# Performance work log

Measured on AMD Instinct MI355X. Metric: run time of the kernel, lower is better.

Reference implementation:

```python
import jax, jax.numpy as jnp
import numpy as np

N = 30000      # nodes
E = 480000     # edges (before self-loops)
D = 100        # hidden_dim / in_channels
H = 4          # heads
PH = 100       # per-head dim
L = 6          # layers
G = 128        # graphs in batch
NUM_ATOM = 100
OUT_DIM = 64


def _xavier(k, shape, gain=1.0):
    fan_in, fan_out = shape[-1], shape[-2]
    lim = gain * np.sqrt(6.0 / (fan_in + fan_out))
    return jax.random.uniform(k, shape, jnp.float32, -lim, lim)


def setup_inputs() -> dict:
    key = jax.random.key(0)
    ks = jax.random.split(key, 12)
    x = jax.random.randint(ks[0], (N,), 0, NUM_ATOM)
    edge_index = jax.random.randint(ks[1], (2, E), 0, N)
    edge_attr = jax.random.normal(ks[2], (E, D), dtype=jnp.float32)
    batch = jnp.sort(jax.random.randint(ks[3], (N,), 0, G))
    emb = _xavier(ks[4], (NUM_ATOM, D))
    W = _xavier(ks[5], (L, H * PH, D))
    We = _xavier(ks[6], (L, H * PH, D))
    a = _xavier(ks[7], (L, H, 2 * PH), gain=1.414)
    ln_g = jnp.ones((L, D), jnp.float32)
    ln_b = jnp.zeros((L, D), jnp.float32)
    w1 = _xavier(ks[8], (OUT_DIM, D))
    b1 = jnp.zeros((OUT_DIM,), jnp.float32)
    w2 = _xavier(ks[9], (1, OUT_DIM))
    b2 = jnp.zeros((1,), jnp.float32)
    return dict(x=x, edge_index=edge_index, edge_attr=edge_attr, batch=batch,
                emb=emb, W=W, We=We, a=a, ln_g=ln_g, ln_b=ln_b,
                w1=w1, b1=b1, w2=w2, b2=b2)


def _forward(x, edge_index, edge_attr, batch, emb, W, We, a, ln_g, ln_b, w1, b1, w2, b2):
    n = x.shape[0]
    loop = jnp.arange(n)
    src = jnp.concatenate([edge_index[0], loop])            # [E']
    dst = jnp.concatenate([edge_index[1], loop])            # [E']  (target, softmax key)
    ea = jnp.concatenate([edge_attr, jnp.zeros((n, D), edge_attr.dtype)], axis=0)  # self-loop attr = 0
    h = emb[x]                                              # [N, D]
    for l in range(L):
        hx = (h @ W[l].T).reshape(n, H, PH)                 # [N, H, PH]
        he = (ea @ We[l].T).reshape(-1, H, PH)              # [E', H, PH]
        a_i, a_j = a[l][:, :PH], a[l][:, PH:]               # [H, PH] each
        # alpha = sum(a * [x_i ; x_j + edge_attr]) split into two dots
        score_i = jnp.einsum('nhd,hd->nh', hx, a_i)         # [N, H]
        xj = hx[src]                                        # [E', H, PH]
        alpha = score_i[dst] + jnp.einsum('ehd,hd->eh', xj + he, a_j)  # [E', H]
        alpha = jnp.where(alpha > 0, alpha, 0.2 * alpha)    # leaky_relu(0.2)
        # segment softmax over edges grouped by target node (every node has a self-loop)
        amax = jax.ops.segment_max(alpha, dst, num_segments=n)
        alpha = jnp.exp(alpha - amax[dst])
        denom = jax.ops.segment_sum(alpha, dst, num_segments=n)
        alpha = alpha / (denom[dst] + 1e-16)
        msg = (xj * alpha[..., None]).sum(axis=1)           # [E', PH] (heads summed, per module)
        aggr = jax.ops.segment_sum(msg, dst, num_segments=n)  # [N, PH]
        # LayerNorm(D), eps=1e-5
        mu = aggr.mean(-1, keepdims=True)
        var = ((aggr - mu) ** 2).mean(-1, keepdims=True)
        y = (aggr - mu) / jnp.sqrt(var + 1e-5) * ln_g[l] + ln_b[l]
        y = jax.nn.elu(y)                                   # dropout = identity (eval)
        h = y + h
    # global mean pool over graphs
    s = jax.ops.segment_sum(h, batch, num_segments=G)
    cnt = jax.ops.segment_sum(jnp.ones((n, 1), h.dtype), batch, num_segments=G)
    pooled = s / jnp.maximum(cnt, 1.0)
    hh = pooled @ w1.T + b1                                 # [G, 64]
    out = hh @ w2.T + b2                                    # [G, 1]
    return out, hh


def reference(x, edge_index, edge_attr, batch, emb, W, We, a, ln_g, ln_b, w1, b1, w2, b2):
    return _forward(x, edge_index, edge_attr, batch, emb, W, We, a, ln_g, ln_b, w1, b1, w2, b2)
```

## Files before the change

kernel.cpp:

```cpp
#include <hip/hip_runtime.h>
#include <cstdint>
#include <cstddef>

#define N_NODES 30000
#define N_EDGES 480000
#define EP_EDGES (N_EDGES + N_NODES)
#define DIM 100
#define NH 4
#define NL 6
#define NG 128
#define KP 416

#define OFF_H       0u
#define OFF_AGG2    12000000u
#define OFF_EID     12000000u
#define OFF_DEG     14040000u
#define OFF_CURS    14160000u
#define OFF_ETMP    16000000u
#define OFF_POOL    12000000u
#define OFF_CNT     12051200u
#define OFF_H16     40000000u
#define OFF_SCI     60000000u
#define OFF_SCJ     60480000u
#define OFF_ESC     60960000u
#define OFF_CWIJ    85440000u
#define OFF_WR      85469184u
#define OFF_INDPTR  86429184u
#define OFF_CSRS    86549248u
#define OFF_BSUM    88589248u
#define OFF_BW      88589376u

typedef _Float16 half8 __attribute__((ext_vector_type(8)));
typedef __fp16 fp16x2 __attribute__((ext_vector_type(2)));
typedef float f32x4 __attribute__((ext_vector_type(4)));

static __device__ __forceinline__ unsigned short f2h(float f) {
  return __builtin_bit_cast(unsigned short, (_Float16)f);
}
static __device__ __forceinline__ float h2f(unsigned short u) {
  return (float)__builtin_bit_cast(_Float16, u);
}

__global__ __launch_bounds__(256) void k_init(const int* __restrict__ x,
                                              const float* __restrict__ emb,
                                              float* __restrict__ h,
                                              unsigned short* __restrict__ h16,
                                              int* __restrict__ deg, int* __restrict__ cursor) {
  int tid = blockIdx.x * 256 + threadIdx.x;
  if (tid < N_NODES * DIM) {
    int n = tid / DIM;
    int d = tid - n * DIM;
    float v = emb[x[n] * DIM + d];
    h[tid] = v;
    h16[tid] = f2h(v);
  }
  if (tid < N_NODES) { deg[tid] = 0; cursor[tid] = 0; }
}

__global__ __launch_bounds__(256) void k_fold(const float* __restrict__ W,
                                              const float* __restrict__ We,
                                              const float* __restrict__ a,
                                              float* __restrict__ cWij,
                                              unsigned short* __restrict__ Bw) {
  int tid = blockIdx.x * 256 + threadIdx.x;
  if (tid < NL * DIM * 8) {
    int l = tid / 800, r = tid % 800;
    int k = r >> 3, c = r & 7;
    int hh = c & 3, isJ = c >> 2;
    const float* wp = W + (size_t)(l * 400 + hh * 100) * 100 + k;
    const float* ap = a + (size_t)(l * 4 + hh) * 200 + isJ * 100;
    float s = 0.f;
    for (int d = 0; d < 100; ++d) s += wp[(size_t)d * 100] * ap[d];
    cWij[l * 800 + k * 8 + c] = s;
  } else if (tid < NL * DIM * 8 + DIM * 24) {
    int m = tid - NL * DIM * 8;
    int k = m / 24, c = m % 24;
    int l = c >> 2, hh = c & 3;
    const float* wp = We + (size_t)(l * 400 + hh * 100) * 100 + k;
    const float* ap = a + (size_t)(l * 4 + hh) * 200 + 100;
    float s = 0.f;
    for (int d = 0; d < 100; ++d) s += wp[(size_t)d * 100] * ap[d];
    _Float16 vh = (_Float16)s;
    _Float16 vl = (_Float16)(s - (float)vh);
    int ct = c >> 4;
    int lane = (((k & 31) >> 3) << 4) | (c & 15);
    int ks = k >> 5;
    int j = k & 7;
    Bw[(size_t)(((0 * 2 + ct) * 4 + ks) * 64 + lane) * 8 + j] = __builtin_bit_cast(unsigned short, vh);
    Bw[(size_t)(((1 * 2 + ct) * 4 + ks) * 64 + lane) * 8 + j] = __builtin_bit_cast(unsigned short, vl);
  } else if (tid < NL * DIM * 8 + DIM * 24 + 8192) {
    int E = tid - (NL * DIM * 8 + DIM * 24);
    int j = E & 7;
    int lane = (E >> 3) & 63;
    int rest = E >> 9;
    int ks = rest & 3;
    int ct = (rest >> 2) & 1;
    int c = ct * 16 + (lane & 15);
    int k = ks * 32 + ((lane >> 4) << 3) + j;
    if (!(c < 24 && k < 100)) Bw[E] = 0;
  }
}

__global__ __launch_bounds__(256) void k_bfrag(const float* __restrict__ W,
                                               unsigned short* __restrict__ Bfrag) {
  int tid = blockIdx.x * 256 + threadIdx.x;
  if (tid >= NL * 7 * 13 * 64 * 8) return;
  int j = tid & 7;
  int lane = (tid >> 3) & 63;
  int rest = tid >> 9;
  int ks = rest % 13;
  int rest2 = rest / 13;
  int ct = rest2 % 7;
  int l = rest2 / 7;
  int k = ks * 32 + ((lane >> 4) << 3) + j;
  int n = ct * 16 + (lane & 15);
  float v = 0.f;
  if (k < 400 && n < 100) {
    int hh = k / 100, kk = k - hh * 100;
    v = W[(size_t)(l * 400 + hh * 100 + n) * 100 + kk];
  }
  Bfrag[tid] = f2h(v);
}

__global__ __launch_bounds__(256) void k_deg(const int* __restrict__ ei, int* __restrict__ deg) {
  int tid = blockIdx.x * 256 + threadIdx.x;
  if (tid >= EP_EDGES) return;
  int dstn = (tid < N_EDGES) ? ei[N_EDGES + tid] : (tid - N_EDGES);
  atomicAdd(&deg[dstn], 1);
}

__global__ __launch_bounds__(1024) void k_scan1(const int* __restrict__ deg,
                                                int* __restrict__ indptr, int* __restrict__ bsum) {
  __shared__ int s[1024];
  int t = threadIdx.x;
  int i = blockIdx.x * 1024 + t;
  int v = (i < N_NODES) ? deg[i] : 0;
  s[t] = v;
  __syncthreads();
  for (int off = 1; off < 1024; off <<= 1) {
    int tmp = (t >= off) ? s[t - off] : 0;
    __syncthreads();
    s[t] += tmp;
    __syncthreads();
  }
  if (i < N_NODES) indptr[i + 1] = s[t];
  if (t == 1023) bsum[blockIdx.x] = s[1023];
}
__global__ __launch_bounds__(64) void k_scan2(int* __restrict__ bsum) {
  int t = threadIdx.x;
  int v = (t < 30) ? bsum[t] : 0;
  int inc = v;
  for (int off = 1; off < 64; off <<= 1) {
    int up = __shfl_up(inc, off);
    if (t >= off) inc += up;
  }
  if (t < 30) bsum[t] = inc - v;
}
__global__ __launch_bounds__(1024) void k_scan3(int* __restrict__ indptr,
                                                const int* __restrict__ bsum) {
  int i = blockIdx.x * 1024 + threadIdx.x;
  if (i < N_NODES) indptr[i + 1] += bsum[blockIdx.x];
  if (i == 0) indptr[0] = 0;
}

__global__ __launch_bounds__(256) void k_scatter(const int* __restrict__ ei,
                                                 const int* __restrict__ indptr,
                                                 int* __restrict__ cursor,
                                                 int* __restrict__ csr_src,
                                                 int* __restrict__ csr_eid) {
  int tid = blockIdx.x * 256 + threadIdx.x;
  if (tid >= EP_EDGES) return;
  int dstn = (tid < N_EDGES) ? ei[N_EDGES + tid] : (tid - N_EDGES);
  int srcn = (tid < N_EDGES) ? ei[tid] : (tid - N_EDGES);
  int p = indptr[dstn] + atomicAdd(&cursor[dstn], 1);
  csr_src[p] = srcn;
  csr_eid[p] = (tid < N_EDGES) ? tid : -1;
}

__global__ __launch_bounds__(256, 4) void k_escore(const float* __restrict__ ea,
                                                   const unsigned short* __restrict__ Bw,
                                                   unsigned short* __restrict__ esc_tmp) {
  __shared__ __align__(16) float s_ea[64 * 128];
  int t = threadIdx.x;
  int lane = t & 63;
  int wv = t >> 6;

  const half8* bp = (const half8*)Bw;
  half8 Bh[2][4], Bl[2][4];
#pragma unroll
  for (int ct = 0; ct < 2; ++ct)
#pragma unroll
    for (int ks = 0; ks < 4; ++ks) {
      Bh[ct][ks] = bp[((0 * 2 + ct) * 4 + ks) * 64 + lane];
      Bl[ct][ks] = bp[((1 * 2 + ct) * 4 + ks) * 64 + lane];
    }

  int e0 = blockIdx.x * 64;
  const float4* g4 = (const float4*)(ea + (size_t)e0 * 100);
  for (int z = t; z < 448; z += 256) {
    int zr = z / 7, zc = z - zr * 7;
    int o = 400 + zc * 16;
    *(float4*)((char*)s_ea + zr * 512 + (o ^ ((zr & 7) << 4))) = (float4){0.f, 0.f, 0.f, 0.f};
  }
#pragma unroll
  for (int i = 0; i < 7; ++i) {
    int v = i * 256 + t;
    if (i < 6 || v < 1600) {
      float4 val = g4[v];
      int r = v / 25, kk = v - r * 25;
      *(float4*)((char*)s_ea + r * 512 + ((kk * 16) ^ ((r & 7) << 4))) = val;
    }
  }
  __syncthreads();

  int c = lane & 15;
  int quad = lane >> 4;
  int lrow = wv * 16 + c;
  int swz = (lrow & 7) << 4;
  const char* base = (const char*)s_ea + lrow * 512;
  f32x4 acc0 = (f32x4){0.f, 0.f, 0.f, 0.f};
  f32x4 acc1 = (f32x4){0.f, 0.f, 0.f, 0.f};
#pragma unroll
  for (int ks = 0; ks < 4; ++ks) {
    int o = ks * 128 + quad * 32;
    float4 xa = *(const float4*)(base + ((o) ^ swz));
    float4 xb = *(const float4*)(base + ((o + 16) ^ swz));
    fp16x2 h0 = __builtin_amdgcn_cvt_pkrtz(xa.x, xa.y);
    fp16x2 h1 = __builtin_amdgcn_cvt_pkrtz(xa.z, xa.w);
    fp16x2 h2 = __builtin_amdgcn_cvt_pkrtz(xb.x, xb.y);
    fp16x2 h3 = __builtin_amdgcn_cvt_pkrtz(xb.z, xb.w);
    fp16x2 l0 = __builtin_amdgcn_cvt_pkrtz(xa.x - (float)h0[0], xa.y - (float)h0[1]);
    fp16x2 l1 = __builtin_amdgcn_cvt_pkrtz(xa.z - (float)h1[0], xa.w - (float)h1[1]);
    fp16x2 l2 = __builtin_amdgcn_cvt_pkrtz(xb.x - (float)h2[0], xb.y - (float)h2[1]);
    fp16x2 l3 = __builtin_amdgcn_cvt_pkrtz(xb.z - (float)h3[0], xb.w - (float)h3[1]);
    uint4 uh = {__builtin_bit_cast(unsigned, h0), __builtin_bit_cast(unsigned, h1),
                __builtin_bit_cast(unsigned, h2), __builtin_bit_cast(unsigned, h3)};
    uint4 ul = {__builtin_bit_cast(unsigned, l0), __builtin_bit_cast(unsigned, l1),
                __builtin_bit_cast(unsigned, l2), __builtin_bit_cast(unsigned, l3)};
    half8 xh = __builtin_bit_cast(half8, uh);
    half8 xl = __builtin_bit_cast(half8, ul);
    acc0 = __builtin_amdgcn_mfma_f32_16x16x32_f16(xh, Bh[0][ks], acc0, 0, 0, 0);
    acc0 = __builtin_amdgcn_mfma_f32_16x16x32_f16(xl, Bh[0][ks], acc0, 0, 0, 0);
    acc0 = __builtin_amdgcn_mfma_f32_16x16x32_f16(xh, Bl[0][ks], acc0, 0, 0, 0);
    acc1 = __builtin_amdgcn_mfma_f32_16x16x32_f16(xh, Bh[1][ks], acc1, 0, 0, 0);
    acc1 = __builtin_amdgcn_mfma_f32_16x16x32_f16(xl, Bh[1][ks], acc1, 0, 0, 0);
    acc1 = __builtin_amdgcn_mfma_f32_16x16x32_f16(xh, Bl[1][ks], acc1, 0, 0, 0);
  }

  unsigned short* orow = esc_tmp + (size_t)(e0 + wv * 16 + quad * 4) * 24;
#pragma unroll
  for (int r = 0; r < 4; ++r) {
    unsigned short* op = orow + r * 24;
    op[c] = f2h(acc0[r]);
    if (c < 8) op[16 + c] = f2h(acc1[r]);
  }
}

__global__ __launch_bounds__(256) void k_permute(const unsigned short* __restrict__ esc_tmp,
                                                 const int* __restrict__ csr_eid,
                                                 unsigned short* __restrict__ esc) {
  int p = blockIdx.x * 256 + threadIdx.x;
  if (p >= EP_EDGES) return;
  int e = csr_eid[p];
  ushort4 v[NL];
  if (e >= 0) {
    const unsigned short* rp = esc_tmp + (size_t)e * 24;
#pragma unroll
    for (int l = 0; l < NL; ++l) v[l] = *(const ushort4*)(rp + l * 4);
  } else {
#pragma unroll
    for (int l = 0; l < NL; ++l) { v[l].x = 0; v[l].y = 0; v[l].z = 0; v[l].w = 0; }
  }
#pragma unroll
  for (int l = 0; l < NL; ++l)
    *(ushort4*)(esc + ((size_t)l * EP_EDGES + p) * 4) = v[l];
}

__global__ __launch_bounds__(256) void k_score(const float* __restrict__ h,
                                               const float* __restrict__ cw,
                                               float* __restrict__ sc_i, float* __restrict__ sc_j) {
  __shared__ __align__(16) float s[DIM * 8];
  for (int i = threadIdx.x; i < DIM * 8; i += 256) s[i] = cw[i];
  __syncthreads();
  int n = blockIdx.x * 256 + threadIdx.x;
  if (n >= N_NODES) return;
  float acc[8] = {0.f, 0.f, 0.f, 0.f, 0.f, 0.f, 0.f, 0.f};
  const float* hr = h + (size_t)n * DIM;
  for (int k4 = 0; k4 < 25; ++k4) {
    float4 v = *(const float4*)(hr + k4 * 4);
    float vv[4] = {v.x, v.y, v.z, v.w};
#pragma unroll
    for (int kk = 0; kk < 4; ++kk) {
      const float* sr = s + (k4 * 4 + kk) * 8;
#pragma unroll
      for (int c = 0; c < 8; ++c) acc[c] += vv[kk] * sr[c];
    }
  }
  *(float4*)(sc_i + (size_t)n * 4) = make_float4(acc[0], acc[1], acc[2], acc[3]);
  *(float4*)(sc_j + (size_t)n * 4) = make_float4(acc[4], acc[5], acc[6], acc[7]);
}

#define ALPHA_P(pp)                                                                  \
  int s_ = csr_src[pp];                                                              \
  float4 sj_ = *(const float4*)(sc_j + (size_t)s_ * 4);                              \
  ushort4 eb_ = *(const ushort4*)(esc_l + (size_t)(pp) * 4);                         \
  float a0 = si.x + sj_.x + h2f(eb_.x); a0 = a0 > 0.f ? a0 : 0.2f * a0;              \
  float a1 = si.y + sj_.y + h2f(eb_.y); a1 = a1 > 0.f ? a1 : 0.2f * a1;              \
  float a2 = si.z + sj_.z + h2f(eb_.z); a2 = a2 > 0.f ? a2 : 0.2f * a2;              \
  float a3 = si.w + sj_.w + h2f(eb_.w); a3 = a3 > 0.f ? a3 : 0.2f * a3;

__global__ __launch_bounds__(256) void k_aggr(const unsigned short* __restrict__ h16,
                                              const float* __restrict__ sc_i,
                                              const float* __restrict__ sc_j,
                                              const unsigned short* __restrict__ esc_l,
                                              const int* __restrict__ indptr,
                                              const int* __restrict__ csr_src,
                                              unsigned short* __restrict__ agg2h) {
  __shared__ __align__(16) uint4 s_pack[4][64];
  int wave = threadIdx.x >> 6;
  int lane = threadIdx.x & 63;
  int n = blockIdx.x * 4 + wave;
  int start = indptr[n], end = indptr[n + 1];
  int deg = end - start;
  float4 si = *(const float4*)(sc_i + (size_t)n * 4);
  float A0 = 0.f, A1 = 0.f, A2 = 0.f, A3 = 0.f;
  float B0 = 0.f, B1 = 0.f, B2 = 0.f, B3 = 0.f;
  bool hasd = lane < 50;

  if (deg <= 64) {
    int p = start + lane;
    bool act = p < end;
    int srcr = 0;
    float a0 = -1e30f, a1 = -1e30f, a2 = -1e30f, a3 = -1e30f;
    if (act) {
      int s2 = csr_src[p];
      float4 sj2 = *(const float4*)(sc_j + (size_t)s2 * 4);
      ushort4 eb2 = *(const ushort4*)(esc_l + (size_t)p * 4);
      a0 = si.x + sj2.x + h2f(eb2.x); a0 = a0 > 0.f ? a0 : 0.2f * a0;
      a1 = si.y + sj2.y + h2f(eb2.y); a1 = a1 > 0.f ? a1 : 0.2f * a1;
      a2 = si.z + sj2.z + h2f(eb2.z); a2 = a2 > 0.f ? a2 : 0.2f * a2;
      a3 = si.w + sj2.w + h2f(eb2.w); a3 = a3 > 0.f ? a3 : 0.2f * a3;
      srcr = s2;
    }
    float m0 = a0, m1 = a1, m2 = a2, m3 = a3;
    for (int off = 32; off; off >>= 1) {
      m0 = fmaxf(m0, __shfl_xor(m0, off));
      m1 = fmaxf(m1, __shfl_xor(m1, off));
      m2 = fmaxf(m2, __shfl_xor(m2, off));
      m3 = fmaxf(m3, __shfl_xor(m3, off));
    }
    float e0 = act ? __expf(a0 - m0) : 0.f;
    float e1 = act ? __expf(a1 - m1) : 0.f;
    float e2 = act ? __expf(a2 - m2) : 0.f;
    float e3 = act ? __expf(a3 - m3) : 0.f;
    float d0 = e0, d1 = e1, d2 = e2, d3 = e3;
    for (int off = 32; off; off >>= 1) {
      d0 += __shfl_xor(d0, off); d1 += __shfl_xor(d1, off);
      d2 += __shfl_xor(d2, off); d3 += __shfl_xor(d3, off);
    }
    float w0 = e0 * (1.f / (d0 + 1e-16f));
    float w1 = e1 * (1.f / (d1 + 1e-16f));
    float w2 = e2 * (1.f / (d2 + 1e-16f));
    float w3 = e3 * (1.f / (d3 + 1e-16f));
    uint4 pk;
    pk.x = (unsigned)srcr;
    pk.y = (unsigned)f2h(w0) | ((unsigned)f2h(w1) << 16);
    pk.z = (unsigned)f2h(w2) | ((unsigned)f2h(w3) << 16);
    pk.w = 0u;
    s_pack[wave][lane] = pk;

    int jm = deg - 1;
    uint4 cp0 = s_pack[wave][0];
    uint4 cp1 = s_pack[wave][min(1, jm)];
    uint4 cp2 = s_pack[wave][min(2, jm)];
    unsigned v0 = hasd ? ((const unsigned*)(h16 + (size_t)cp0.x * DIM))[lane] : 0u;
    unsigned v1 = hasd ? ((const unsigned*)(h16 + (size_t)cp1.x * DIM))[lane] : 0u;
    unsigned v2 = hasd ? ((const unsigned*)(h16 + (size_t)cp2.x * DIM))[lane] : 0u;
#pragma unroll 3
    for (int j = 0; j < deg; ++j) {
      uint4 cpn = s_pack[wave][min(j + 3, jm)];
      unsigned vn = hasd ? ((const unsigned*)(h16 + (size_t)cpn.x * DIM))[lane] : 0u;
      float q0 = h2f((unsigned short)(cp0.y & 0xffffu));
      float q1 = h2f((unsigned short)(cp0.y >> 16));
      float q2 = h2f((unsigned short)(cp0.z & 0xffffu));
      float q3 = h2f((unsigned short)(cp0.z >> 16));
      float he = h2f((unsigned short)(v0 & 0xffffu));
      float ho = h2f((unsigned short)(v0 >> 16));
      A0 += q0 * he; A1 += q1 * he; A2 += q2 * he; A3 += q3 * he;
      B0 += q0 * ho; B1 += q1 * ho; B2 += q2 * ho; B3 += q3 * ho;
      cp0 = cp1; v0 = v1;
      cp1 = cp2; v1 = v2;
      cp2 = cpn; v2 = vn;
    }
  } else {
    float m0 = -1e30f, m1 = -1e30f, m2 = -1e30f, m3 = -1e30f;
    for (int p = start + lane; p < end; p += 64) {
      ALPHA_P(p)
      (void)s_;
      m0 = fmaxf(m0, a0); m1 = fmaxf(m1, a1); m2 = fmaxf(m2, a2); m3 = fmaxf(m3, a3);
    }
    for (int off = 32; off; off >>= 1) {
      m0 = fmaxf(m0, __shfl_xor(m0, off));
      m1 = fmaxf(m1, __shfl_xor(m1, off));
      m2 = fmaxf(m2, __shfl_xor(m2, off));
      m3 = fmaxf(m3, __shfl_xor(m3, off));
    }
    float d0 = 0.f, d1 = 0.f, d2 = 0.f, d3 = 0.f;
    for (int p = start + lane; p < end; p += 64) {
      ALPHA_P(p)
      (void)s_;
      d0 += __expf(a0 - m0); d1 += __expf(a1 - m1);
      d2 += __expf(a2 - m2); d3 += __expf(a3 - m3);
    }
    for (int off = 32; off; off >>= 1) {
      d0 += __shfl_xor(d0, off); d1 += __shfl_xor(d1, off);
      d2 += __shfl_xor(d2, off); d3 += __shfl_xor(d3, off);
    }
    float i0 = 1.f / (d0 + 1e-16f), i1 = 1.f / (d1 + 1e-16f);
    float i2 = 1.f / (d2 + 1e-16f), i3 = 1.f / (d3 + 1e-16f);
    for (int base = start; base < end; base += 64) {
      int cntv = min(64, end - base);
      int p = base + lane;
      float w0 = 0.f, w1 = 0.f, w2 = 0.f, w3 = 0.f;
      int srcr = 0;
      if (p < end) {
        ALPHA_P(p)
        w0 = __expf(a0 - m0) * i0; w1 = __expf(a1 - m1) * i1;
        w2 = __expf(a2 - m2) * i2; w3 = __expf(a3 - m3) * i3;
        srcr = s_;
      }
      for (int j = 0; j < cntv; ++j) {
        int sj2 = __shfl(srcr, j);
        float q0 = __shfl(w0, j), q1 = __shfl(w1, j);
        float q2 = __shfl(w2, j), q3 = __shfl(w3, j);
        unsigned hv = hasd ? ((const unsigned*)(h16 + (size_t)sj2 * DIM))[lane] : 0u;
        float he = h2f((unsigned short)(hv & 0xffffu));
        float ho = h2f((unsigned short)(hv >> 16));
        A0 += q0 * he; A1 += q1 * he; A2 += q2 * he; A3 += q3 * he;
        B0 += q0 * ho; B1 += q1 * ho; B2 += q2 * ho; B3 += q3 * ho;
      }
    }
  }
  unsigned short* outp = agg2h + (size_t)n * KP;
  if (hasd) {
    *(unsigned*)(outp + 2 * lane)       = (unsigned)f2h(A0) | ((unsigned)f2h(B0) << 16);
    *(unsigned*)(outp + 100 + 2 * lane) = (unsigned)f2h(A1) | ((unsigned)f2h(B1) << 16);
    *(unsigned*)(outp + 200 + 2 * lane) = (unsigned)f2h(A2) | ((unsigned)f2h(B2) << 16);
    *(unsigned*)(outp + 300 + 2 * lane) = (unsigned)f2h(A3) | ((unsigned)f2h(B3) << 16);
  }
  if (lane < KP - 400) outp[400 + lane] = 0;
}

__global__ __launch_bounds__(256) void k_gemm2(const _Float16* __restrict__ agg2h,
                                               const _Float16* __restrict__ Bfrag_l,
                                               const float* __restrict__ lg,
                                               const float* __restrict__ lb,
                                               float* __restrict__ h,
                                               unsigned short* __restrict__ h16) {
  int t = threadIdx.x;
  int lane = t & 63;
  int w = t >> 6;
  int c = lane & 15;
  int quad = lane >> 4;
  int nb = blockIdx.x * 64 + w * 16;

  f32x4 acc[7];
#pragma unroll
  for (int ct = 0; ct < 7; ++ct) acc[ct] = (f32x4){0.f, 0.f, 0.f, 0.f};

  const _Float16* arow = agg2h + (size_t)(nb + c) * KP + quad * 8;
#pragma unroll
  for (int ks = 0; ks < 13; ++ks) {
    half8 a = *(const half8*)(arow + ks * 32);
    const _Float16* bp = Bfrag_l + (size_t)(ks * 64 + lane) * 8;
#pragma unroll
    for (int ct = 0; ct < 7; ++ct) {
      half8 b = *(const half8*)(bp + (size_t)ct * 13 * 64 * 8);
      acc[ct] = __builtin_amdgcn_mfma_f32_16x16x32_f16(a, b, acc[ct], 0, 0, 0);
    }
  }

  float gv[7], bv[7];
#pragma unroll
  for (int ct = 0; ct < 7; ++ct) {
    int col = ct * 16 + c;
    gv[ct] = (col < DIM) ? lg[col] : 0.f;
    bv[ct] = (col < DIM) ? lb[col] : 0.f;
  }
  bool c4 = c < 4;
#pragma unroll
  for (int r = 0; r < 4; ++r) {
    int n = nb + quad * 4 + r;
    float v[7];
#pragma unroll
    for (int ct = 0; ct < 7; ++ct) v[ct] = acc[ct][r];
    float s = v[0] + v[1] + v[2] + v[3] + v[4] + v[5] + (c4 ? v[6] : 0.f);
    s += __shfl_xor(s, 1); s += __shfl_xor(s, 2);
    s += __shfl_xor(s, 4); s += __shfl_xor(s, 8);
    float mu = s * 0.01f;
    float dv[7];
    float s2 = 0.f;
#pragma unroll
    for (int ct = 0; ct < 6; ++ct) { dv[ct] = v[ct] - mu; s2 += dv[ct] * dv[ct]; }
    dv[6] = c4 ? (v[6] - mu) : 0.f;
    s2 += dv[6] * dv[6];
    s2 += __shfl_xor(s2, 1); s2 += __shfl_xor(s2, 2);
    s2 += __shfl_xor(s2, 4); s2 += __shfl_xor(s2, 8);
    float rstd = rsqrtf(s2 * 0.01f + 1e-5f);
    if (n < N_NODES) {
      float* hp = h + (size_t)n * DIM;
      unsigned short* hp16 = h16 + (size_t)n * DIM;
#pragma unroll
      for (int ct = 0; ct < 7; ++ct) {
        int col = ct * 16 + c;
        if (ct < 6 || c4) {
          float y = dv[ct] * rstd * gv[ct] + bv[ct];
          y = y > 0.f ? y : (__expf(y) - 1.f);
          float nh = hp[col] + y;
          hp[col] = nh;
          hp16[col] = f2h(nh);
        }
      }
    }
  }
}

__global__ __launch_bounds__(128) void k_pool(const float* __restrict__ h,
                                              const int* __restrict__ batch,
                                              float* __restrict__ pooled, float* __restrict__ cnt) {
  int d = threadIdx.x;
  int n0 = blockIdx.x * 64;
  int n1 = min(n0 + 64, N_NODES);
  if (n0 >= N_NODES) return;
  int curg = -1;
  float acc = 0.f, c = 0.f;
  for (int n = n0; n < n1; ++n) {
    int g = batch[n];
    if (g != curg) {
      if (curg >= 0) {
        if (d < 100) atomicAdd(&pooled[(size_t)curg * DIM + d], acc);
        if (d == 0) atomicAdd(&cnt[curg], c);
      }
      curg = g; acc = 0.f; c = 0.f;
    }
    if (d < 100) acc += h[(size_t)n * DIM + d];
    c += 1.f;
  }
  if (curg >= 0) {
    if (d < 100) atomicAdd(&pooled[(size_t)curg * DIM + d], acc);
    if (d == 0) atomicAdd(&cnt[curg], c);
  }
}

__global__ __launch_bounds__(64) void k_mlp(const float* __restrict__ pooled,
                                            const float* __restrict__ cnt,
                                            const float* __restrict__ w1, const float* __restrict__ b1,
                                            const float* __restrict__ w2, const float* __restrict__ b2,
                                            float* __restrict__ out) {
  int g = blockIdx.x;
  int j = threadIdx.x;
  float invc = 1.0f / fmaxf(cnt[g], 1.0f);
  const float* pr = pooled + (size_t)g * DIM;
  const float* wr = w1 + (size_t)j * DIM;
  float acc = 0.f;
  for (int k = 0; k < DIM; ++k) acc += pr[k] * wr[k];
  float hh = acc * invc + b1[j];
  out[NG + g * 64 + j] = hh;
  float v = hh * w2[j];
  for (int off = 32; off; off >>= 1) v += __shfl_xor(v, off);
  if (j == 0) out[g] = v + b2[0];
}

extern "C" void kernel_launch(void* const* d_in, const int* in_sizes, int n_in,
                              void* d_out, int out_size, void* d_ws, size_t ws_size,
                              hipStream_t stream) {
  (void)in_sizes; (void)n_in; (void)out_size; (void)ws_size;
  const int* x = (const int*)d_in[0];
  const int* ei = (const int*)d_in[1];
  const float* ea = (const float*)d_in[2];
  const int* batch = (const int*)d_in[3];
  const float* emb = (const float*)d_in[4];
  const float* W = (const float*)d_in[5];
  const float* We = (const float*)d_in[6];
  const float* a = (const float*)d_in[7];
  const float* ln_g = (const float*)d_in[8];
  const float* ln_b = (const float*)d_in[9];
  const float* w1 = (const float*)d_in[10];
  const float* b1 = (const float*)d_in[11];
  const float* w2 = (const float*)d_in[12];
  const float* b2 = (const float*)d_in[13];
  float* outp = (float*)d_out;

  char* ws = (char*)d_ws;
  float* h = (float*)(ws + OFF_H);
  unsigned short* agg2h = (unsigned short*)(ws + OFF_AGG2);
  int* csr_eid = (int*)(ws + OFF_EID);
  int* deg = (int*)(ws + OFF_DEG);
  int* cursor = (int*)(ws + OFF_CURS);
  unsigned short* esc_tmp = (unsigned short*)(ws + OFF_ETMP);
  float* pooled = (float*)(ws + OFF_POOL);
  float* cnt = (float*)(ws + OFF_CNT);
  unsigned short* h16 = (unsigned short*)(ws + OFF_H16);
  float* sc_i = (float*)(ws + OFF_SCI);
  float* sc_j = (float*)(ws + OFF_SCJ);
  unsigned short* esc = (unsigned short*)(ws + OFF_ESC);
  float* cWij = (float*)(ws + OFF_CWIJ);
  unsigned short* Bw = (unsigned short*)(ws + OFF_BW);
  unsigned short* Bfrag = (unsigned short*)(ws + OFF_WR);
  int* indptr = (int*)(ws + OFF_INDPTR);
  int* csr_src = (int*)(ws + OFF_CSRS);
  int* bsum = (int*)(ws + OFF_BSUM);

  k_init<<<11719, 256, 0, stream>>>(x, emb, h, h16, deg, cursor);
  k_fold<<<61, 256, 0, stream>>>(W, We, a, cWij, Bw);
  k_bfrag<<<1092, 256, 0, stream>>>(W, Bfrag);
  k_deg<<<1993, 256, 0, stream>>>(ei, deg);
  k_scan1<<<30, 1024, 0, stream>>>(deg, indptr, bsum);
  k_scan2<<<1, 64, 0, stream>>>(bsum);
  k_scan3<<<30, 1024, 0, stream>>>(indptr, bsum);
  k_scatter<<<1993, 256, 0, stream>>>(ei, indptr, cursor, csr_src, csr_eid);
  k_escore<<<7500, 256, 0, stream>>>(ea, Bw, esc_tmp);
  k_permute<<<1993, 256, 0, stream>>>(esc_tmp, csr_eid, esc);

  for (int l = 0; l < NL; ++l) {
    k_score<<<118, 256, 0, stream>>>(h, cWij + l * 800, sc_i, sc_j);
    k_aggr<<<7500, 256, 0, stream>>>(h16, sc_i, sc_j, esc + (size_t)l * EP_EDGES * 4,
                                     indptr, csr_src, agg2h);
    k_gemm2<<<469, 256, 0, stream>>>((const _Float16*)agg2h,
                                     (const _Float16*)(Bfrag + (size_t)l * 7 * 13 * 64 * 8),
                                     ln_g + l * 100, ln_b + l * 100, h, h16);
  }

  hipMemsetAsync(ws + OFF_POOL, 0, 51200 + 512, stream);
  k_pool<<<469, 128, 0, stream>>>(h, batch, pooled, cnt);
  k_mlp<<<128, 64, 0, stream>>>(pooled, cnt, w1, b1, w2, b2, outp);
}
```

Baseline: 827.6 us.

## Merge setup kernels and fuse next-layer score into GEMM epilogue

```diff
diff --git a/kernel.cpp b/kernel.cpp
--- a/kernel.cpp
+++ b/kernel.cpp
@@ -30,6 +30,11 @@
 #define OFF_BSUM    88589248u
 #define OFF_BW      88589376u
 
+#define T_INIT  (N_NODES * DIM)
+#define T_BFRAG (NL * 7 * 13 * 64 * 8)
+#define T_FOLD  (NL * DIM * 8 + DIM * 24 + 8192)
+#define T_ALL   (T_INIT + T_BFRAG + T_FOLD + EP_EDGES)
+
 typedef _Float16 half8 __attribute__((ext_vector_type(8)));
 typedef __fp16 fp16x2 __attribute__((ext_vector_type(2)));
 typedef float f32x4 __attribute__((ext_vector_type(4)));
@@ -41,92 +46,91 @@
   return (float)__builtin_bit_cast(_Float16, u);
 }
 
-__global__ __launch_bounds__(256) void k_init(const int* __restrict__ x,
+__global__ __launch_bounds__(256) void k_mega(const int* __restrict__ x,
                                               const float* __restrict__ emb,
+                                              const int* __restrict__ ei,
+                                              const float* __restrict__ W,
+                                              const float* __restrict__ We,
+                                              const float* __restrict__ a,
                                               float* __restrict__ h,
                                               unsigned short* __restrict__ h16,
-                                              int* __restrict__ deg, int* __restrict__ cursor) {
+                                              unsigned short* __restrict__ Bfrag,
+                                              float* __restrict__ cWij,
+                                              unsigned short* __restrict__ Bw,
+                                              int* __restrict__ deg) {
   int tid = blockIdx.x * 256 + threadIdx.x;
-  if (tid < N_NODES * DIM) {
+  if (tid < T_INIT) {
     int n = tid / DIM;
     int d = tid - n * DIM;
     float v = emb[x[n] * DIM + d];
     h[tid] = v;
     h16[tid] = f2h(v);
-  }
-  if (tid < N_NODES) { deg[tid] = 0; cursor[tid] = 0; }
-}
-
-__global__ __launch_bounds__(256) void k_fold(const float* __restrict__ W,
-                                              const float* __restrict__ We,
-                                              const float* __restrict__ a,
-                                              float* __restrict__ cWij,
-                                              unsigned short* __restrict__ Bw) {
-  int tid = blockIdx.x * 256 + threadIdx.x;
-  if (tid < NL * DIM * 8) {
-    int l = tid / 800, r = tid % 800;
-    int k = r >> 3, c = r & 7;
-    int hh = c & 3, isJ = c >> 2;
-    const float* wp = W + (size_t)(l * 400 + hh * 100) * 100 + k;
-    const float* ap = a + (size_t)(l * 4 + hh) * 200 + isJ * 100;
-    float s = 0.f;
-    for (int d = 0; d < 100; ++d) s += wp[(size_t)d * 100] * ap[d];
-    cWij[l * 800 + k * 8 + c] = s;
-  } else if (tid < NL * DIM * 8 + DIM * 24) {
-    int m = tid - NL * DIM * 8;
-    int k = m / 24, c = m % 24;
-    int l = c >> 2, hh = c & 3;
-    const float* wp = We + (size_t)(l * 400 + hh * 100) * 100 + k;
-    const float* ap = a + (size_t)(l * 4 + hh) * 200 + 100;
-    float s = 0.f;
-    for (int d = 0; d < 100; ++d) s += wp[(size_t)d * 100] * ap[d];
-    _Float16 vh = (_Float16)s;
-    _Float16 vl = (_Float16)(s - (float)vh);
-    int ct = c >> 4;
-    int lane = (((k & 31) >> 3) << 4) | (c & 15);
-    int ks = k >> 5;
-    int j = k & 7;
-    Bw[(size_t)(((0 * 2 + ct) * 4 + ks) * 64 + lane) * 8 + j] = __builtin_bit_cast(unsigned short, vh);
-    Bw[(size_t)(((1 * 2 + ct) * 4 + ks) * 64 + lane) * 8 + j] = __builtin_bit_cast(unsigned short, vl);
-  } else if (tid < NL * DIM * 8 + DIM * 24 + 8192) {
-    int E = tid - (NL * DIM * 8 + DIM * 24);
-    int j = E & 7;
-    int lane = (E >> 3) & 63;
-    int rest = E >> 9;
-    int ks = rest & 3;
-    int ct = (rest >> 2) & 1;
-    int c = ct * 16 + (lane & 15);
+    return;
+  }
+  tid -= T_INIT;
+  if (tid < T_BFRAG) {
+    int j = tid & 7;
+    int lane = (tid >> 3) & 63;
+    int rest = tid >> 9;
+    int ks = rest % 13;
+    int rest2 = rest / 13;
+    int ct = rest2 % 7;
+    int l = rest2 / 7;
     int k = ks * 32 + ((lane >> 4) << 3) + j;
-    if (!(c < 24 && k < 100)) Bw[E] = 0;
-  }
-}
-
-__global__ __launch_bounds__(256) void k_bfrag(const float* __restrict__ W,
-                                               unsigned short* __restrict__ Bfrag) {
-  int tid = blockIdx.x * 256 + threadIdx.x;
-  if (tid >= NL * 7 * 13 * 64 * 8) return;
-  int j = tid & 7;
-  int lane = (tid >> 3) & 63;
-  int rest = tid >> 9;
-  int ks = rest % 13;
-  int rest2 = rest / 13;
-  int ct = rest2 % 7;
-  int l = rest2 / 7;
-  int k = ks * 32 + ((lane >> 4) << 3) + j;
-  int n = ct * 16 + (lane & 15);
-  float v = 0.f;
-  if (k < 400 && n < 100) {
-    int hh = k / 100, kk = k - hh * 100;
-    v = W[(size_t)(l * 400 + hh * 100 + n) * 100 + kk];
-  }
-  Bfrag[tid] = f2h(v);
-}
-
-__global__ __launch_bounds__(256) void k_deg(const int* __restrict__ ei, int* __restrict__ deg) {
-  int tid = blockIdx.x * 256 + threadIdx.x;
-  if (tid >= EP_EDGES) return;
-  int dstn = (tid < N_EDGES) ? ei[N_EDGES + tid] : (tid - N_EDGES);
-  atomicAdd(&deg[dstn], 1);
+    int n = ct * 16 + (lane & 15);
+    float v = 0.f;
+    if (k < 400 && n < 100) {
+      int hh = k / 100, kk = k - hh * 100;
+      v = W[(size_t)(l * 400 + hh * 100 + n) * 100 + kk];
+    }
+    Bfrag[tid] = f2h(v);
+    return;
+  }
+  tid -= T_BFRAG;
+  if (tid < T_FOLD) {
+    if (tid < NL * DIM * 8) {
+      int l = tid / 800, r = tid % 800;
+      int k = r >> 3, c = r & 7;
+      int hh = c & 3, isJ = c >> 2;
+      const float* wp = W + (size_t)(l * 400 + hh * 100) * 100 + k;
+      const float* ap = a + (size_t)(l * 4 + hh) * 200 + isJ * 100;
+      float s = 0.f;
+      for (int d = 0; d < 100; ++d) s += wp[(size_t)d * 100] * ap[d];
+      cWij[l * 800 + k * 8 + c] = s;
+    } else if (tid < NL * DIM * 8 + DIM * 24) {
+      int m = tid - NL * DIM * 8;
+      int k = m / 24, c = m % 24;
+      int l = c >> 2, hh = c & 3;
+      const float* wp = We + (size_t)(l * 400 + hh * 100) * 100 + k;
+      const float* ap = a + (size_t)(l * 4 + hh) * 200 + 100;
+      float s = 0.f;
+      for (int d = 0; d < 100; ++d) s += wp[(size_t)d * 100] * ap[d];
+      _Float16 vh = (_Float16)s;
+      _Float16 vl = (_Float16)(s - (float)vh);
+      int ct = c >> 4;
+      int lane = (((k & 31) >> 3) << 4) | (c & 15);
+      int ks = k >> 5;
+      int j = k & 7;
+      Bw[(size_t)(((0 * 2 + ct) * 4 + ks) * 64 + lane) * 8 + j] = __builtin_bit_cast(unsigned short, vh);
+      Bw[(size_t)(((1 * 2 + ct) * 4 + ks) * 64 + lane) * 8 + j] = __builtin_bit_cast(unsigned short, vl);
+    } else {
+      int E = tid - (NL * DIM * 8 + DIM * 24);
+      int j = E & 7;
+      int lane = (E >> 3) & 63;
+      int rest = E >> 9;
+      int ks = rest & 3;
+      int ct = (rest >> 2) & 1;
+      int c = ct * 16 + (lane & 15);
+      int k = ks * 32 + ((lane >> 4) << 3) + j;
+      if (!(c < 24 && k < 100)) Bw[E] = 0;
+    }
+    return;
+  }
+  tid -= T_FOLD;
+  if (tid < EP_EDGES) {
+    int dstn = (tid < N_EDGES) ? ei[N_EDGES + tid] : (tid - N_EDGES);
+    atomicAdd(&deg[dstn], 1);
+  }
 }
 
 __global__ __launch_bounds__(1024) void k_scan1(const int* __restrict__ deg,
@@ -146,20 +150,18 @@
   if (i < N_NODES) indptr[i + 1] = s[t];
   if (t == 1023) bsum[blockIdx.x] = s[1023];
 }
-__global__ __launch_bounds__(64) void k_scan2(int* __restrict__ bsum) {
-  int t = threadIdx.x;
-  int v = (t < 30) ? bsum[t] : 0;
-  int inc = v;
-  for (int off = 1; off < 64; off <<= 1) {
-    int up = __shfl_up(inc, off);
-    if (t >= off) inc += up;
-  }
-  if (t < 30) bsum[t] = inc - v;
-}
 __global__ __launch_bounds__(1024) void k_scan3(int* __restrict__ indptr,
                                                 const int* __restrict__ bsum) {
-  int i = blockIdx.x * 1024 + threadIdx.x;
-  if (i < N_NODES) indptr[i + 1] += bsum[blockIdx.x];
+  __shared__ int soff;
+  int t = threadIdx.x;
+  if (t < 64) {
+    int v = (t < 30 && t < blockIdx.x) ? bsum[t] : 0;
+    for (int off = 32; off; off >>= 1) v += __shfl_xor(v, off);
+    if (t == 0) soff = v;
+  }
+  __syncthreads();
+  int i = blockIdx.x * 1024 + t;
+  if (i < N_NODES) indptr[i + 1] += soff;
   if (i == 0) indptr[0] = 0;
 }
 
@@ -456,8 +458,16 @@
                                                const float* __restrict__ lg,
                                                const float* __restrict__ lb,
                                                float* __restrict__ h,
-                                               unsigned short* __restrict__ h16) {
+                                               unsigned short* __restrict__ h16,
+                                               const float* __restrict__ cw_next,
+                                               float* __restrict__ sc_i,
+                                               float* __restrict__ sc_j,
+                                               int do_score) {
+  __shared__ __align__(16) float s_cw[896];
   int t = threadIdx.x;
+  for (int i = t; i < 896; i += 256) s_cw[i] = (i < 800) ? cw_next[i] : 0.f;
+  __syncthreads();
+
   int lane = t & 63;
   int w = t >> 6;
   int c = lane & 15;
@@ -507,6 +517,9 @@
     s2 += __shfl_xor(s2, 1); s2 += __shfl_xor(s2, 2);
     s2 += __shfl_xor(s2, 4); s2 += __shfl_xor(s2, 8);
     float rstd = rsqrtf(s2 * 0.01f + 1e-5f);
+    float nh[7];
+#pragma unroll
+    for (int ct = 0; ct < 7; ++ct) nh[ct] = 0.f;
     if (n < N_NODES) {
       float* hp = h + (size_t)n * DIM;
       unsigned short* hp16 = h16 + (size_t)n * DIM;
@@ -516,10 +529,33 @@
         if (ct < 6 || c4) {
           float y = dv[ct] * rstd * gv[ct] + bv[ct];
           y = y > 0.f ? y : (__expf(y) - 1.f);
-          float nh = hp[col] + y;
-          hp[col] = nh;
-          hp16[col] = f2h(nh);
+          float vnh = hp[col] + y;
+          hp[col] = vnh;
+          hp16[col] = f2h(vnh);
+          nh[ct] = vnh;
         }
+      }
+    }
+    if (do_score) {
+      float sa[8] = {0.f, 0.f, 0.f, 0.f, 0.f, 0.f, 0.f, 0.f};
+#pragma unroll
+      for (int ct = 0; ct < 7; ++ct) {
+        const float4* wr = (const float4*)(s_cw + (ct * 16 + c) * 8);
+        float4 wA = wr[0], wB = wr[1];
+        float x = nh[ct];
+        sa[0] += x * wA.x; sa[1] += x * wA.y; sa[2] += x * wA.z; sa[3] += x * wA.w;
+        sa[4] += x * wB.x; sa[5] += x * wB.y; sa[6] += x * wB.z; sa[7] += x * wB.w;
+      }
+#pragma unroll
+      for (int k = 0; k < 8; ++k) {
+        sa[k] += __shfl_xor(sa[k], 1);
+        sa[k] += __shfl_xor(sa[k], 2);
+        sa[k] += __shfl_xor(sa[k], 4);
+        sa[k] += __shfl_xor(sa[k], 8);
+      }
+      if (c == 0 && n < N_NODES) {
+        *(float4*)(sc_i + (size_t)n * 4) = make_float4(sa[0], sa[1], sa[2], sa[3]);
+        *(float4*)(sc_j + (size_t)n * 4) = make_float4(sa[4], sa[5], sa[6], sa[7]);
       }
     }
   }
@@ -611,24 +647,24 @@
   int* csr_src = (int*)(ws + OFF_CSRS);
   int* bsum = (int*)(ws + OFF_BSUM);
 
-  k_init<<<11719, 256, 0, stream>>>(x, emb, h, h16, deg, cursor);
-  k_fold<<<61, 256, 0, stream>>>(W, We, a, cWij, Bw);
-  k_bfrag<<<1092, 256, 0, stream>>>(W, Bfrag);
-  k_deg<<<1993, 256, 0, stream>>>(ei, deg);
+  hipMemsetAsync(ws + OFF_DEG, 0, 240000, stream);
+  k_mega<<<(T_ALL + 255) / 256, 256, 0, stream>>>(x, emb, ei, W, We, a,
+                                                  h, h16, Bfrag, cWij, Bw, deg);
   k_scan1<<<30, 1024, 0, stream>>>(deg, indptr, bsum);
-  k_scan2<<<1, 64, 0, stream>>>(bsum);
   k_scan3<<<30, 1024, 0, stream>>>(indptr, bsum);
   k_scatter<<<1993, 256, 0, stream>>>(ei, indptr, cursor, csr_src, csr_eid);
   k_escore<<<7500, 256, 0, stream>>>(ea, Bw, esc_tmp);
   k_permute<<<1993, 256, 0, stream>>>(esc_tmp, csr_eid, esc);
+  k_score<<<118, 256, 0, stream>>>(h, cWij, sc_i, sc_j);
 
   for (int l = 0; l < NL; ++l) {
-    k_score<<<118, 256, 0, stream>>>(h, cWij + l * 800, sc_i, sc_j);
     k_aggr<<<7500, 256, 0, stream>>>(h16, sc_i, sc_j, esc + (size_t)l * EP_EDGES * 4,
                                      indptr, csr_src, agg2h);
+    int nl = (l + 1 < NL) ? (l + 1) : 0;
     k_gemm2<<<469, 256, 0, stream>>>((const _Float16*)agg2h,
                                      (const _Float16*)(Bfrag + (size_t)l * 7 * 13 * 64 * 8),
-                                     ln_g + l * 100, ln_b + l * 100, h, h16);
+                                     ln_g + l * 100, ln_b + l * 100, h, h16,
+                                     cWij + nl * 800, sc_i, sc_j, (l + 1 < NL) ? 1 : 0);
   }
 
   hipMemsetAsync(ws + OFF_POOL, 0, 51200 + 512, stream);
```

New measurement: 930.9 us. 12.5% more time.
